# Kernel optimization log

Hardware: AMD Instinct MI355X
Metric: run time of the kernel (lower is better)

The kernel has to match this reference:

```python
import math
import jax, jax.numpy as jnp
import numpy as np

B, N, D, H, NI, NL, NS, MID = 32, 2048, 256, 8, 64, 3, 32, 3


def _ln(x, g, b, eps=1e-5):
    m = jnp.mean(x, axis=-1, keepdims=True)
    v = jnp.mean((x - m) ** 2, axis=-1, keepdims=True)
    return (x - m) * jax.lax.rsqrt(v + eps) * g + b


def _mab(Q, K, mask, Wq, bq, Wk, bk, Wv, bv, Wo, bo, g0, b0, g1, b1):
    # torch's split(dim_split,2)+cat(...,0) == reshape to (B, n, H, dh)
    dh = D // H
    q = (Q @ Wq + bq).reshape(Q.shape[0], Q.shape[1], H, dh)
    k = (K @ Wk + bk).reshape(K.shape[0], K.shape[1], H, dh)
    v = (K @ Wv + bv).reshape(K.shape[0], K.shape[1], H, dh)
    A = jnp.einsum('bqhd,bkhd->bhqk', q, k) / math.sqrt(D)  # note: sqrt(dim_V), faithful
    A = jnp.where(mask[:, None, None, :] == 0, -1e4, A)
    A = jax.nn.softmax(A, axis=-1)
    o = q + jnp.einsum('bhqk,bkhd->bqhd', A, v)
    O = o.reshape(Q.shape[0], Q.shape[1], D)
    O = _ln(O, g0, b0)
    O = O + jax.nn.relu(O @ Wo + bo)
    return _ln(O, g1, b1)


def _forward(x_values, y_target, point_mask, proj_W, proj_b, isab_I,
             isab_Wq, isab_bq, isab_Wk, isab_bk, isab_Wv, isab_bv,
             isab_Wo, isab_bo, isab_g0, isab_b0, isab_g1, isab_b1,
             pma_S, pma_Wq, pma_bq, pma_Wk, pma_bk, pma_Wv, pma_bv,
             pma_Wo, pma_bo, pma_g0, pma_b0, pma_g1, pma_b1):
    # input_dim == max_input_dim, so the zero-padded feature build is a concat
    feats = jnp.concatenate([x_values, y_target[..., None]], axis=-1)  # (B, N, MID+1)
    x = jax.nn.gelu(feats @ proj_W + proj_b, approximate=False)
    ones_mask = jnp.ones((x.shape[0], NI), jnp.float32)
    stk = (isab_Wq, isab_bq, isab_Wk, isab_bk, isab_Wv, isab_bv,
           isab_Wo, isab_bo, isab_g0, isab_b0, isab_g1, isab_b1)
    for l in range(NL):
        I = jnp.broadcast_to(isab_I[l][None], (x.shape[0], NI, D))
        h = _mab(I, x, point_mask, *[a[l, 0] for a in stk])   # mab0: inducing pts attend to X
        x = _mab(x, h, ones_mask, *[a[l, 1] for a in stk])    # mab1: X attends to H (all valid)
    S = jnp.broadcast_to(pma_S[None], (x.shape[0], NS, D))
    return _mab(S, x, point_mask, pma_Wq, pma_bq, pma_Wk, pma_bk, pma_Wv,
                pma_bv, pma_Wo, pma_bo, pma_g0, pma_b0, pma_g1, pma_b1)


def setup_inputs():
    key = jax.random.key(0)
    ks = iter(jax.random.split(key, 40))
    def nrm(shape, s=0.05):
        return jax.random.normal(next(ks), shape, dtype=jnp.float32) * s
    z = lambda shape: jnp.zeros(shape, jnp.float32)
    o = lambda shape: jnp.ones(shape, jnp.float32)
    return {
        'x_values': jax.random.normal(next(ks), (B, N, MID), jnp.float32),
        'y_target': jax.random.normal(next(ks), (B, N), jnp.float32),
        'point_mask': jax.random.randint(next(ks), (B, N), 0, 2).astype(jnp.float32),
        'proj_W': nrm((MID + 1, D)), 'proj_b': z((D,)),
        'isab_I': nrm((NL, NI, D), 0.1),
        'isab_Wq': nrm((NL, 2, D, D)), 'isab_bq': z((NL, 2, D)),
        'isab_Wk': nrm((NL, 2, D, D)), 'isab_bk': z((NL, 2, D)),
        'isab_Wv': nrm((NL, 2, D, D)), 'isab_bv': z((NL, 2, D)),
        'isab_Wo': nrm((NL, 2, D, D)), 'isab_bo': z((NL, 2, D)),
        'isab_g0': o((NL, 2, D)), 'isab_b0': z((NL, 2, D)),
        'isab_g1': o((NL, 2, D)), 'isab_b1': z((NL, 2, D)),
        'pma_S': nrm((NS, D), 0.1),
        'pma_Wq': nrm((D, D)), 'pma_bq': z((D,)),
        'pma_Wk': nrm((D, D)), 'pma_bk': z((D,)),
        'pma_Wv': nrm((D, D)), 'pma_bv': z((D,)),
        'pma_Wo': nrm((D, D)), 'pma_bo': z((D,)),
        'pma_g0': o((D,)), 'pma_b0': z((D,)),
        'pma_g1': o((D,)), 'pma_b1': z((D,)),
    }


def reference(x_values, y_target, point_mask, proj_W, proj_b, isab_I,
              isab_Wq, isab_bq, isab_Wk, isab_bk, isab_Wv, isab_bv,
              isab_Wo, isab_bo, isab_g0, isab_b0, isab_g1, isab_b1,
              pma_S, pma_Wq, pma_bq, pma_Wk, pma_bk, pma_Wv, pma_bv,
              pma_Wo, pma_bo, pma_g0, pma_b0, pma_g1, pma_b1):
    return _forward(x_values, y_target, point_mask, proj_W, proj_b, isab_I,
                    isab_Wq, isab_bq, isab_Wk, isab_bk, isab_Wv, isab_bv,
                    isab_Wo, isab_bo, isab_g0, isab_b0, isab_g1, isab_b1,
                    pma_S, pma_Wq, pma_bq, pma_Wk, pma_bk, pma_Wv, pma_bv,
                    pma_Wo, pma_bo, pma_g0, pma_b0, pma_g1, pma_b1)
```

## Files before the change

kernel.cpp:

```cpp
#include <hip/hip_runtime.h>
#include <hip/hip_bf16.h>


typedef __attribute__((ext_vector_type(8))) short short8;
typedef __attribute__((ext_vector_type(4))) float f32x4;
typedef __attribute__((ext_vector_type(4))) ushort ushort4v;

__device__ __forceinline__ ushort f2bf(float f) {
  uint u = __builtin_bit_cast(uint, f);
  u += 0x7fffu + ((u >> 16) & 1u);
  return (ushort)(u >> 16);
}
__device__ __forceinline__ float bf2f(ushort h) {
  uint u = (uint)h << 16;
  return __builtin_bit_cast(float, u);
}

__global__ __launch_bounds__(256) void prep_weights(
    const float* __restrict__ Wq, const float* __restrict__ Wk,
    const float* __restrict__ Wv, const float* __restrict__ Wo,
    const float* __restrict__ pWq, const float* __restrict__ pWk,
    const float* __restrict__ pWv, const float* __restrict__ pWo,
    ushort* __restrict__ wt)
{
  __shared__ float tile[64][65];
  const int m = blockIdx.y;
  const int t = blockIdx.x;
  const int tr = (t >> 2) * 64;
  const int tc = (t & 3) * 64;
  const float* src;
  if (m < 24) {
    int l = m >> 3, s = (m >> 2) & 1, w = m & 3;
    const float* base = (w == 0) ? Wq : (w == 1) ? Wk : (w == 2) ? Wv : Wo;
    src = base + (size_t)(l * 2 + s) * 65536;
  } else {
    int w = m & 3;
    src = (w == 0) ? pWq : (w == 1) ? pWk : (w == 2) ? pWv : pWo;
  }
  const int tid = threadIdx.x;
  const int cn = tid & 63;
  const int rk = tid >> 6;
#pragma unroll
  for (int j = 0; j < 16; ++j) {
    int kl = rk + j * 4;
    tile[kl][cn] = src[(size_t)(tr + kl) * 256 + tc + cn];
  }
  __syncthreads();
  ushort* dst = wt + (size_t)m * 65536;
#pragma unroll
  for (int j = 0; j < 16; ++j) {
    int nl = rk + j * 4;
    dst[(size_t)(tc + nl) * 256 + tr + cn] = f2bf(tile[cn][nl]);
  }
}

__global__ __launch_bounds__(256) void proj_gelu(
    const float* __restrict__ xv, const float* __restrict__ yt,
    const float* __restrict__ pW, const float* __restrict__ pb,
    ushort* __restrict__ xb)
{
  const int d = threadIdx.x;
  const int row0 = blockIdx.x * 8;
  const float w0 = pW[d], w1 = pW[256 + d], w2 = pW[512 + d], w3 = pW[768 + d];
  const float bz = pb[d];
#pragma unroll
  for (int rr = 0; rr < 8; ++rr) {
    int row = row0 + rr;
    float f0 = xv[(size_t)row * 3 + 0];
    float f1 = xv[(size_t)row * 3 + 1];
    float f2 = xv[(size_t)row * 3 + 2];
    float f3 = yt[row];
    float a = bz + f0 * w0 + f1 * w1 + f2 * w2 + f3 * w3;
    float g = 0.5f * a * (1.f + erff(a * 0.70710678118654752f));
    xb[(size_t)row * 256 + d] = f2bf(g);
  }
}

__global__ __launch_bounds__(256) void gemm_q(
    const float* __restrict__ iI, const float* __restrict__ pS,
    const ushort* __restrict__ wt, const float* __restrict__ ibq,
    const float* __restrict__ pbq, ushort* __restrict__ q_all)
{
  const int bq = blockIdx.x;
  const float* A; const ushort* Wt; const float* bias; ushort* out; int M;
  if (bq < 3) { A = iI + bq * 16384; Wt = wt + (size_t)(bq * 8) * 65536; bias = ibq + bq * 512; out = q_all + bq * 16384; M = 64; }
  else        { A = pS; Wt = wt + (size_t)24 * 65536; bias = pbq; out = q_all + 49152; M = 32; }
  const int tid = threadIdx.x;
  const int wave = tid >> 6, lane = tid & 63;
  const int l15 = lane & 15, l4 = lane >> 4, koff = l4 * 8;
  f32x4 acc[4][4];
#pragma unroll
  for (int i = 0; i < 4; ++i)
#pragma unroll
    for (int j = 0; j < 4; ++j) acc[i][j] = (f32x4)0.f;
#pragma unroll
  for (int ks = 0; ks < 8; ++ks) {
    short8 af[4];
#pragma unroll
    for (int mf = 0; mf < 4; ++mf) {
      if (mf * 16 < M) {
        const float* ap = A + (size_t)(mf * 16 + l15) * 256 + ks * 32 + koff;
        float4 f0 = *(const float4*)ap;
        float4 f1 = *(const float4*)(ap + 4);
        short8 sv;
        sv[0] = (short)f2bf(f0.x); sv[1] = (short)f2bf(f0.y);
        sv[2] = (short)f2bf(f0.z); sv[3] = (short)f2bf(f0.w);
        sv[4] = (short)f2bf(f1.x); sv[5] = (short)f2bf(f1.y);
        sv[6] = (short)f2bf(f1.z); sv[7] = (short)f2bf(f1.w);
        af[mf] = sv;
      } else af[mf] = (short8)0;
    }
#pragma unroll
    for (int nf = 0; nf < 4; ++nf) {
      short8 bf = *(const short8*)(Wt + (size_t)(wave * 64 + nf * 16 + l15) * 256 + ks * 32 + koff);
#pragma unroll
      for (int mf = 0; mf < 4; ++mf)
        acc[mf][nf] = __builtin_amdgcn_mfma_f32_16x16x32_bf16(af[mf], bf, acc[mf][nf], 0, 0, 0);
    }
  }
#pragma unroll
  for (int mf = 0; mf < 4; ++mf) {
    if (mf * 16 >= M) continue;
#pragma unroll
    for (int nf = 0; nf < 4; ++nf) {
      int col = wave * 64 + nf * 16 + l15;
      float bcol = bias[col];
#pragma unroll
      for (int r = 0; r < 4; ++r)
        out[(size_t)(mf * 16 + l4 * 4 + r) * 256 + col] = f2bf(acc[mf][nf][r] + bcol);
    }
  }
}

template <int EPI, bool OUTF32, int COLS>
__global__ __launch_bounds__(COLS * 2, (COLS == 128) ? 4 : 2) void gemm_bp(
    const ushort* __restrict__ A,
    const ushort* __restrict__ Wt0, const ushort* __restrict__ Wt1, const ushort* __restrict__ Wt2,
    const float* __restrict__ b0, const float* __restrict__ b1, const float* __restrict__ b2,
    void* __restrict__ o0, void* __restrict__ o1, void* __restrict__ o2,
    const float* __restrict__ lng, const float* __restrict__ lnb,
    int ny, int nyz)
{
  constexpr int WC = COLS / 64;
  constexpr int PS = COLS * 64;
  constexpr int ROWB = COLS * 2;
  __shared__ __align__(16) char Bs[4 * PS];
  __shared__ float redbuf[(EPI == 3) ? 1280 : 4];
  const int bid = blockIdx.x;
  const int rest = bid >> 3;
  const int yz = rest % nyz;
  const int bx = ((rest / nyz) << 3) | (bid & 7);
  const int y = yz % ny;
  const int z = yz / ny;
  const ushort* Wt = (z == 0) ? Wt0 : ((z == 1) ? Wt1 : Wt2);
  const float* bias = (z == 0) ? b0 : ((z == 1) ? b1 : b2);
  void* outp = (z == 0) ? o0 : ((z == 1) ? o1 : o2);
  const int pcol = y * COLS;

  const int tid = threadIdx.x;
  const int wave = tid >> 6, lane = tid & 63;
  const int wc = wave % WC, wr = wave / WC;
  const int l15 = lane & 15, l4 = lane >> 4;
  const int row0 = bx * 128;
  const int sn = tid >> 1, sseg = tid & 1;

  f32x4 acc[4][4];
#pragma unroll
  for (int i = 0; i < 4; ++i)
#pragma unroll
    for (int j = 0; j < 4; ++j) acc[i][j] = (f32x4)0.f;

#pragma unroll
  for (int half = 0; half < 2; ++half) {
    if (half) __syncthreads();
    {
      const ushort* src = Wt + (size_t)(pcol + sn) * 256 + half * 128 + sseg * 64;
#pragma unroll
      for (int c = 0; c < 8; ++c) {
        uint4 w = *(const uint4*)(src + c * 8);
        int plane = sseg * 2 + (c >> 2);
        char* dst = Bs + plane * PS + sn * 64 + (((c & 3) * 16) ^ (((sn >> 1) & 3) << 4));
        *(uint4*)dst = w;
      }
    }
    __syncthreads();
#pragma unroll
    for (int ks = 0; ks < 4; ++ks) {
      short8 af[4];
#pragma unroll
      for (int mfa = 0; mfa < 4; ++mfa)
        af[mfa] = *(const short8*)(A + (size_t)(row0 + wr * 64 + mfa * 16 + l15) * 256 + half * 128 + ks * 32 + l4 * 8);
#pragma unroll
      for (int nfb = 0; nfb < 4; ++nfb) {
        int n = wc * 64 + nfb * 16 + l15;
        short8 bf = *(const short8*)(Bs + ks * PS + n * 64 + ((l4 * 16) ^ (((n >> 1) & 3) << 4)));
#pragma unroll
        for (int mfa = 0; mfa < 4; ++mfa)
          acc[mfa][nfb] = __builtin_amdgcn_mfma_f32_16x16x32_bf16(bf, af[mfa], acc[mfa][nfb], 0, 0, 0);
      }
    }
  }

  if constexpr (EPI == 0) {
    __syncthreads();
#pragma unroll
    for (int nfb = 0; nfb < 4; ++nfb) {
      f32x4 bv = *(const f32x4*)(bias + pcol + wc * 64 + nfb * 16 + l4 * 4);
      int colb = wc * 128 + nfb * 32 + l4 * 8;
#pragma unroll
      for (int mfa = 0; mfa < 4; ++mfa) {
        int row = wr * 64 + mfa * 16 + l15;
        ushort4v pk;
#pragma unroll
        for (int i = 0; i < 4; ++i) pk[i] = f2bf(acc[mfa][nfb][i] + bv[i]);
        *(ushort4v*)(Bs + row * ROWB + (colb ^ ((row & 7) << 4))) = pk;
      }
    }
    __syncthreads();
    const int srow = tid >> 2, seg = tid & 3;
#pragma unroll
    for (int rr = 0; rr < 2; ++rr) {
      int row = srow + rr * 64;
      int x = (row & 7) << 4;
      ushort* gdst = (ushort*)outp + (size_t)(row0 + row) * 256 + pcol;
#pragma unroll
      for (int it = 0; it < 4; ++it) {
        int colb = seg * 16 + it * 64;
        uint4 v = *(const uint4*)(Bs + row * ROWB + (colb ^ x));
        *(uint4*)(gdst + colb / 2) = v;
      }
    }
  } else {
    float* red1 = redbuf;
    float* red2 = redbuf + 512;
    float* mv_ = redbuf + 1024;
    float* rv_ = redbuf + 1152;
    float s1[4] = {0.f, 0.f, 0.f, 0.f}, s2[4] = {0.f, 0.f, 0.f, 0.f};
#pragma unroll
    for (int nfb = 0; nfb < 4; ++nfb) {
      int col0 = wc * 64 + nfb * 16 + l4 * 4;
      f32x4 bv = *(const f32x4*)(bias + col0);
#pragma unroll
      for (int mfa = 0; mfa < 4; ++mfa) {
        size_t row = (size_t)row0 + wr * 64 + mfa * 16 + l15;
        ushort4v rz = *(const ushort4v*)(A + row * 256 + col0);
#pragma unroll
        for (int i = 0; i < 4; ++i) {
          float zz = bf2f(rz[i]) + fmaxf(acc[mfa][nfb][i] + bv[i], 0.f);
          acc[mfa][nfb][i] = zz;
          s1[mfa] += zz;
          s2[mfa] += zz * zz;
        }
      }
    }
#pragma unroll
    for (int mfa = 0; mfa < 4; ++mfa) {
      s1[mfa] += __shfl_xor(s1[mfa], 16); s1[mfa] += __shfl_xor(s1[mfa], 32);
      s2[mfa] += __shfl_xor(s2[mfa], 16); s2[mfa] += __shfl_xor(s2[mfa], 32);
    }
    if (l4 == 0) {
#pragma unroll
      for (int mfa = 0; mfa < 4; ++mfa) {
        red1[wc * 128 + wr * 64 + mfa * 16 + l15] = s1[mfa];
        red2[wc * 128 + wr * 64 + mfa * 16 + l15] = s2[mfa];
      }
    }
    __syncthreads();
    if (tid < 128) {
      float m1 = red1[tid] + red1[128 + tid] + red1[256 + tid] + red1[384 + tid];
      float m2 = red2[tid] + red2[128 + tid] + red2[256 + tid] + red2[384 + tid];
      float mean = m1 * 0.00390625f;
      float var = m2 * 0.00390625f - mean * mean;
      mv_[tid] = mean;
      rv_[tid] = rsqrtf(var + 1e-5f);
    }
    __syncthreads();
#pragma unroll
    for (int nfb = 0; nfb < 4; ++nfb) {
      int col0 = wc * 64 + nfb * 16 + l4 * 4;
      f32x4 gg = *(const f32x4*)(lng + col0);
      f32x4 bb = *(const f32x4*)(lnb + col0);
      int colb = col0 * 2;
#pragma unroll
      for (int mfa = 0; mfa < 4; ++mfa) {
        int lr = wr * 64 + mfa * 16 + l15;
        float mean = mv_[lr], rs = rv_[lr];
        if constexpr (OUTF32) {
          f32x4 w;
#pragma unroll
          for (int i = 0; i < 4; ++i) w[i] = (acc[mfa][nfb][i] - mean) * rs * gg[i] + bb[i];
          *(f32x4*)((float*)outp + ((size_t)row0 + lr) * 256 + col0) = w;
        } else {
          ushort4v pk;
#pragma unroll
          for (int i = 0; i < 4; ++i) pk[i] = f2bf((acc[mfa][nfb][i] - mean) * rs * gg[i] + bb[i]);
          *(ushort4v*)(Bs + lr * ROWB + (colb ^ ((lr & 7) << 4))) = pk;
        }
      }
    }
    if constexpr (!OUTF32) {
      __syncthreads();
      const int srow = tid >> 2, seg = tid & 3;
      int x = (srow & 7) << 4;
      ushort* gdst = (ushort*)outp + (size_t)(row0 + srow) * 256;
#pragma unroll
      for (int it = 0; it < 8; ++it) {
        int colb = seg * 16 + it * 64;
        uint4 v = *(const uint4*)(Bs + srow * ROWB + (colb ^ x));
        *(uint4*)(gdst + colb / 2) = v;
      }
    }
  }
}

template <int MF>
__global__ __launch_bounds__(512) void attn_fused(
    const ushort* __restrict__ qb, const ushort* __restrict__ xbuf,
    const ushort* __restrict__ wk, const float* __restrict__ bk,
    const ushort* __restrict__ wv, const float* __restrict__ bv,
    const float* __restrict__ mask, ushort* __restrict__ O)
{
  __shared__ __align__(16) ushort Ps[8][64][72];
  __shared__ __align__(16) ushort Vt[8][32][72];
  __shared__ __align__(16) ushort Kc[8][64][40];
  const int b = blockIdx.x, h = blockIdx.y;
  const int tid = threadIdx.x;
  const int w = tid >> 6, lane = tid & 63;
  const int l15 = lane & 15, l4 = lane >> 4;
  const int koff = l4 * 8;
  const int kvbase = b * 2048;

  short8 qf[MF];
#pragma unroll
  for (int mf = 0; mf < MF; ++mf)
    qf[mf] = *(const short8*)(qb + (size_t)(mf * 16 + l15) * 256 + h * 32 + koff);

  f32x4 bkv[2], bvv[2];
#pragma unroll
  for (int nfb = 0; nfb < 2; ++nfb) {
    bkv[nfb] = *(const f32x4*)(bk + h * 32 + nfb * 16 + l4 * 4);
    bvv[nfb] = *(const f32x4*)(bv + h * 32 + nfb * 16 + l4 * 4);
  }

  f32x4 Oa[MF][2];
  float Mr[MF][4], Lr[MF][4];
#pragma unroll
  for (int mf = 0; mf < MF; ++mf) {
    Oa[mf][0] = (f32x4)0.f; Oa[mf][1] = (f32x4)0.f;
#pragma unroll
    for (int r = 0; r < 4; ++r) { Mr[mf][r] = -1e30f; Lr[mf][r] = 0.f; }
  }

  for (int c = 0; c < 4; ++c) {
    const int kc = w * 256 + c * 64;
    f32x4 ak[4][2], av[4][2];
#pragma unroll
    for (int i = 0; i < 4; ++i) {
      ak[i][0] = (f32x4)0.f; ak[i][1] = (f32x4)0.f;
      av[i][0] = (f32x4)0.f; av[i][1] = (f32x4)0.f;
    }
#pragma unroll
    for (int ks = 0; ks < 8; ++ks) {
      short8 af[4];
#pragma unroll
      for (int mfa = 0; mfa < 4; ++mfa)
        af[mfa] = *(const short8*)(xbuf + (size_t)(kvbase + kc + mfa * 16 + l15) * 256 + ks * 32 + koff);
#pragma unroll
      for (int nfb = 0; nfb < 2; ++nfb) {
        int n = h * 32 + nfb * 16 + l15;
        short8 wkf = *(const short8*)(wk + (size_t)n * 256 + ks * 32 + koff);
        short8 wvf = *(const short8*)(wv + (size_t)n * 256 + ks * 32 + koff);
#pragma unroll
        for (int mfa = 0; mfa < 4; ++mfa) {
          ak[mfa][nfb] = __builtin_amdgcn_mfma_f32_16x16x32_bf16(wkf, af[mfa], ak[mfa][nfb], 0, 0, 0);
          av[mfa][nfb] = __builtin_amdgcn_mfma_f32_16x16x32_bf16(wvf, af[mfa], av[mfa][nfb], 0, 0, 0);
        }
      }
    }
#pragma unroll
    for (int nfb = 0; nfb < 2; ++nfb)
#pragma unroll
      for (int mfa = 0; mfa < 4; ++mfa) {
        ushort4v pk;
#pragma unroll
        for (int i = 0; i < 4; ++i) pk[i] = f2bf(ak[mfa][nfb][i] + bkv[nfb][i]);
        *(ushort4v*)&Kc[w][mfa * 16 + l15][nfb * 16 + l4 * 4] = pk;
      }
#pragma unroll
    for (int nfb = 0; nfb < 2; ++nfb)
#pragma unroll
      for (int mfa = 0; mfa < 4; ++mfa)
#pragma unroll
        for (int i = 0; i < 4; ++i)
          Vt[w][nfb * 16 + l4 * 4 + i][mfa * 16 + l15] = f2bf(av[mfa][nfb][i] + bvv[nfb][i]);

    f32x4 S[MF][4];
#pragma unroll
    for (int nf = 0; nf < 4; ++nf) {
      short8 kf = *(const short8*)&Kc[w][nf * 16 + l15][koff];
#pragma unroll
      for (int mf = 0; mf < MF; ++mf)
        S[mf][nf] = __builtin_amdgcn_mfma_f32_16x16x32_bf16(qf[mf], kf, (f32x4)0.f, 0, 0, 0);
    }
    float mv[4];
#pragma unroll
    for (int nf = 0; nf < 4; ++nf)
      mv[nf] = mask[(size_t)b * 2048 + kc + nf * 16 + l15];
#pragma unroll
    for (int mf = 0; mf < MF; ++mf)
#pragma unroll
      for (int nf = 0; nf < 4; ++nf)
#pragma unroll
        for (int r = 0; r < 4; ++r) {
          float s = S[mf][nf][r] * 0.0625f;
          S[mf][nf][r] = (mv[nf] != 0.f) ? s : -1e4f;
        }
#pragma unroll
    for (int mf = 0; mf < MF; ++mf)
#pragma unroll
      for (int r = 0; r < 4; ++r) {
        float pm = fmaxf(fmaxf(S[mf][0][r], S[mf][1][r]), fmaxf(S[mf][2][r], S[mf][3][r]));
        pm = fmaxf(pm, __shfl_xor(pm, 1));
        pm = fmaxf(pm, __shfl_xor(pm, 2));
        pm = fmaxf(pm, __shfl_xor(pm, 4));
        pm = fmaxf(pm, __shfl_xor(pm, 8));
        float Mnew = fmaxf(Mr[mf][r], pm);
        float corr = __expf(Mr[mf][r] - Mnew);
        Mr[mf][r] = Mnew;
        float rs = 0.f;
#pragma unroll
        for (int nf = 0; nf < 4; ++nf) {
          float p = __expf(S[mf][nf][r] - Mnew);
          S[mf][nf][r] = p;
          rs += p;
        }
        rs += __shfl_xor(rs, 1);
        rs += __shfl_xor(rs, 2);
        rs += __shfl_xor(rs, 4);
        rs += __shfl_xor(rs, 8);
        Lr[mf][r] = Lr[mf][r] * corr + rs;
        Oa[mf][0][r] *= corr;
        Oa[mf][1][r] *= corr;
      }
#pragma unroll
    for (int mf = 0; mf < MF; ++mf)
#pragma unroll
      for (int nf = 0; nf < 4; ++nf)
#pragma unroll
        for (int r = 0; r < 4; ++r)
          Ps[w][mf * 16 + l4 * 4 + r][nf * 16 + l15] = f2bf(S[mf][nf][r]);
#pragma unroll
    for (int ks = 0; ks < 2; ++ks) {
      short8 pf[MF];
#pragma unroll
      for (int mf = 0; mf < MF; ++mf)
        pf[mf] = *(const short8*)&Ps[w][mf * 16 + l15][ks * 32 + koff];
#pragma unroll
      for (int nf2 = 0; nf2 < 2; ++nf2) {
        short8 vf = *(const short8*)&Vt[w][nf2 * 16 + l15][ks * 32 + koff];
#pragma unroll
        for (int mf = 0; mf < MF; ++mf)
          Oa[mf][nf2] = __builtin_amdgcn_mfma_f32_16x16x32_bf16(pf[mf], vf, Oa[mf][nf2], 0, 0, 0);
      }
    }
  }

  __syncthreads();
  float* Mw = (float*)&Ps[0][0][0];
  float* Lw = Mw + 512;
  float* Ow = Lw + 512;
#pragma unroll
  for (int mf = 0; mf < MF; ++mf)
#pragma unroll
    for (int r = 0; r < 4; ++r) {
      int row = mf * 16 + l4 * 4 + r;
      if (l15 == 0) { Mw[w * 64 + row] = Mr[mf][r]; Lw[w * 64 + row] = Lr[mf][r]; }
#pragma unroll
      for (int nf2 = 0; nf2 < 2; ++nf2)
        Ow[(w * 64 + row) * 33 + nf2 * 16 + l15] = Oa[mf][nf2][r];
    }
  __syncthreads();
  const int NQ = MF * 16;
  int row = tid >> 3, dg = tid & 7;
  if (row < NQ) {
    float mm = -1e30f;
#pragma unroll
    for (int s = 0; s < 8; ++s) mm = fmaxf(mm, Mw[s * 64 + row]);
    float den = 0.f, es[8];
#pragma unroll
    for (int s = 0; s < 8; ++s) {
      es[s] = __expf(Mw[s * 64 + row] - mm);
      den += Lw[s * 64 + row] * es[s];
    }
    float invden = 1.f / den;
    ushort4v pk;
#pragma unroll
    for (int i = 0; i < 4; ++i) {
      int d = dg * 4 + i;
      float num = 0.f;
#pragma unroll
      for (int s = 0; s < 8; ++s) num += Ow[(s * 64 + row) * 33 + d] * es[s];
      float qv = bf2f(qb[(size_t)row * 256 + h * 32 + d]);
      pk[i] = f2bf(qv + num * invden);
    }
    *(ushort4v*)(O + (size_t)(b * NQ + row) * 256 + h * 32 + dg * 4) = pk;
  }
}

__global__ __launch_bounds__(512, 4) void mab1_fused(
    const ushort* __restrict__ xb, const ushort* __restrict__ wq,
    const float* __restrict__ bq,
    const ushort* __restrict__ kb, const ushort* __restrict__ vb,
    const ushort* __restrict__ wo, const float* __restrict__ bo,
    const float* __restrict__ g0, const float* __restrict__ b0v,
    const float* __restrict__ g1, const float* __restrict__ b1v,
    ushort* __restrict__ outb)
{
  __shared__ __align__(16) ushort Qs[8][64][40];
  __shared__ __align__(16) ushort Psh[8][16][40];
  __shared__ __align__(16) ushort Vth[8][32][40];
  __shared__ float red1[8][64], red2[8][64], mv_[64], rv_[64];
  ushort* o_s = &Qs[0][0][0];
  constexpr int OS = 264;

  const int qt = blockIdx.x, b = blockIdx.y;
  const int tid = threadIdx.x;
  const int w = tid >> 6, lane = tid & 63;
  const int l15 = lane & 15, l4 = lane >> 4;
  const int koff = l4 * 8;
  const size_t row0 = (size_t)b * 2048 + qt * 64;
  const int kvbase = b * 64;
  const int h = w;

  short8 kf[4];
#pragma unroll
  for (int nf = 0; nf < 4; ++nf)
    kf[nf] = *(const short8*)(kb + (size_t)(kvbase + nf * 16 + l15) * 256 + h * 32 + koff);
  const int key = lane & 31, dh2 = lane >> 5;
  short8 vvB0, vvB1;
  {
    const ushort* vsrcA = vb + (size_t)(kvbase + key) * 256 + h * 32 + dh2 * 16;
    const ushort* vsrcB = vb + (size_t)(kvbase + 32 + key) * 256 + h * 32 + dh2 * 16;
    short8 vvA0 = *(const short8*)vsrcA;
    short8 vvA1 = *(const short8*)(vsrcA + 8);
    vvB0 = *(const short8*)vsrcB;
    vvB1 = *(const short8*)(vsrcB + 8);
#pragma unroll
    for (int j = 0; j < 8; ++j) Vth[w][dh2 * 16 + j][key] = (ushort)vvA0[j];
#pragma unroll
    for (int j = 0; j < 8; ++j) Vth[w][dh2 * 16 + 8 + j][key] = (ushort)vvA1[j];
  }

  {
    f32x4 qa[4][2];
#pragma unroll
    for (int i = 0; i < 4; ++i) { qa[i][0] = (f32x4)0.f; qa[i][1] = (f32x4)0.f; }
#pragma unroll
    for (int ks = 0; ks < 8; ++ks) {
      short8 af[4];
#pragma unroll
      for (int mfa = 0; mfa < 4; ++mfa)
        af[mfa] = *(const short8*)(xb + (row0 + mfa * 16 + l15) * 256 + ks * 32 + koff);
#pragma unroll
      for (int nfb = 0; nfb < 2; ++nfb) {
        int n = w * 32 + nfb * 16 + l15;
        short8 bf = *(const short8*)(wq + (size_t)n * 256 + ks * 32 + koff);
#pragma unroll
        for (int mfa = 0; mfa < 4; ++mfa)
          qa[mfa][nfb] = __builtin_amdgcn_mfma_f32_16x16x32_bf16(bf, af[mfa], qa[mfa][nfb], 0, 0, 0);
      }
    }
#pragma unroll
    for (int nfb = 0; nfb < 2; ++nfb) {
      f32x4 bvq = *(const f32x4*)(bq + w * 32 + nfb * 16 + l4 * 4);
#pragma unroll
      for (int mfa = 0; mfa < 4; ++mfa) {
        ushort4v pk;
#pragma unroll
        for (int i = 0; i < 4; ++i) pk[i] = f2bf(qa[mfa][nfb][i] + bvq[i]);
        *(ushort4v*)&Qs[w][mfa * 16 + l15][nfb * 16 + l4 * 4] = pk;
      }
    }
  }

  short8 qf[4];
#pragma unroll
  for (int mf = 0; mf < 4; ++mf)
    qf[mf] = *(const short8*)&Qs[w][mf * 16 + l15][koff];

  f32x4 S[4][4];
#pragma unroll
  for (int nf = 0; nf < 4; ++nf) {
#pragma unroll
    for (int mf = 0; mf < 4; ++mf)
      S[mf][nf] = __builtin_amdgcn_mfma_f32_16x16x32_bf16(qf[mf], kf[nf], (f32x4)0.f, 0, 0, 0);
  }
  float Lr[4][4];
#pragma unroll
  for (int mf = 0; mf < 4; ++mf)
#pragma unroll
    for (int r = 0; r < 4; ++r) {
      float pm = fmaxf(fmaxf(S[mf][0][r], S[mf][1][r]), fmaxf(S[mf][2][r], S[mf][3][r])) * 0.0625f;
      pm = fmaxf(pm, __shfl_xor(pm, 1));
      pm = fmaxf(pm, __shfl_xor(pm, 2));
      pm = fmaxf(pm, __shfl_xor(pm, 4));
      pm = fmaxf(pm, __shfl_xor(pm, 8));
      float rs = 0.f;
#pragma unroll
      for (int nf = 0; nf < 4; ++nf) {
        float p = __expf(S[mf][nf][r] * 0.0625f - pm);
        S[mf][nf][r] = p;
        rs += p;
      }
      rs += __shfl_xor(rs, 1);
      rs += __shfl_xor(rs, 2);
      rs += __shfl_xor(rs, 4);
      rs += __shfl_xor(rs, 8);
      Lr[mf][r] = rs;
    }

  f32x4 Oa[4][2];
#pragma unroll
  for (int mf = 0; mf < 4; ++mf) { Oa[mf][0] = (f32x4)0.f; Oa[mf][1] = (f32x4)0.f; }
#pragma unroll
  for (int mf = 0; mf < 4; ++mf) {
#pragma unroll
    for (int nf = 0; nf < 2; ++nf)
#pragma unroll
      for (int r = 0; r < 4; ++r)
        Psh[w][l4 * 4 + r][nf * 16 + l15] = f2bf(S[mf][nf][r]);
    short8 pf = *(const short8*)&Psh[w][l15][koff];
#pragma unroll
    for (int nf2 = 0; nf2 < 2; ++nf2) {
      short8 vf = *(const short8*)&Vth[w][nf2 * 16 + l15][koff];
      Oa[mf][nf2] = __builtin_amdgcn_mfma_f32_16x16x32_bf16(pf, vf, Oa[mf][nf2], 0, 0, 0);
    }
  }
#pragma unroll
  for (int j = 0; j < 8; ++j) Vth[w][dh2 * 16 + j][key] = (ushort)vvB0[j];
#pragma unroll
  for (int j = 0; j < 8; ++j) Vth[w][dh2 * 16 + 8 + j][key] = (ushort)vvB1[j];
#pragma unroll
  for (int mf = 0; mf < 4; ++mf) {
#pragma unroll
    for (int nf = 0; nf < 2; ++nf)
#pragma unroll
      for (int r = 0; r < 4; ++r)
        Psh[w][l4 * 4 + r][nf * 16 + l15] = f2bf(S[mf][nf + 2][r]);
    short8 pf = *(const short8*)&Psh[w][l15][koff];
#pragma unroll
    for (int nf2 = 0; nf2 < 2; ++nf2) {
      short8 vf = *(const short8*)&Vth[w][nf2 * 16 + l15][koff];
      Oa[mf][nf2] = __builtin_amdgcn_mfma_f32_16x16x32_bf16(pf, vf, Oa[mf][nf2], 0, 0, 0);
    }
  }

  {
    float s1[4][4], s2[4][4];
#pragma unroll
    for (int mf = 0; mf < 4; ++mf)
#pragma unroll
      for (int r = 0; r < 4; ++r) {
        float invL = 1.f / Lr[mf][r];
        s1[mf][r] = 0.f; s2[mf][r] = 0.f;
#pragma unroll
        for (int nf2 = 0; nf2 < 2; ++nf2) {
          float qv = bf2f(Qs[w][mf * 16 + l4 * 4 + r][nf2 * 16 + l15]);
          float z = qv + Oa[mf][nf2][r] * invL;
          Oa[mf][nf2][r] = z;
          s1[mf][r] += z;
          s2[mf][r] += z * z;
        }
#pragma unroll
        for (int off = 1; off < 16; off <<= 1) {
          s1[mf][r] += __shfl_xor(s1[mf][r], off);
          s2[mf][r] += __shfl_xor(s2[mf][r], off);
        }
        if (l15 == 0) {
          int row = mf * 16 + l4 * 4 + r;
          red1[w][row] = s1[mf][r];
          red2[w][row] = s2[mf][r];
        }
      }
  }
  __syncthreads();
  if (tid < 64) {
    float m1 = 0.f, m2 = 0.f;
#pragma unroll
    for (int s = 0; s < 8; ++s) { m1 += red1[s][tid]; m2 += red2[s][tid]; }
    float mean = m1 * 0.00390625f;
    float var = m2 * 0.00390625f - mean * mean;
    mv_[tid] = mean;
    rv_[tid] = rsqrtf(var + 1e-5f);
  }
  __syncthreads();
#pragma unroll
  for (int nf2 = 0; nf2 < 2; ++nf2) {
    int col = h * 32 + nf2 * 16 + l15;
    float gc = g0[col], bc = b0v[col];
#pragma unroll
    for (int mf = 0; mf < 4; ++mf)
#pragma unroll
      for (int r = 0; r < 4; ++r) {
        int row = mf * 16 + l4 * 4 + r;
        float v = (Oa[mf][nf2][r] - mv_[row]) * rv_[row] * gc + bc;
        o_s[row * OS + col] = f2bf(v);
      }
  }
  __syncthreads();

  f32x4 oa[4][2];
#pragma unroll
  for (int i = 0; i < 4; ++i) { oa[i][0] = (f32x4)0.f; oa[i][1] = (f32x4)0.f; }
#pragma unroll
  for (int ks = 0; ks < 8; ++ks) {
    short8 af[4];
#pragma unroll
    for (int mfa = 0; mfa < 4; ++mfa)
      af[mfa] = *(const short8*)&o_s[(mfa * 16 + l15) * OS + ks * 32 + koff];
#pragma unroll
    for (int nfb = 0; nfb < 2; ++nfb) {
      int n = w * 32 + nfb * 16 + l15;
      short8 bf = *(const short8*)(wo + (size_t)n * 256 + ks * 32 + koff);
#pragma unroll
      for (int mfa = 0; mfa < 4; ++mfa)
        oa[mfa][nfb] = __builtin_amdgcn_mfma_f32_16x16x32_bf16(bf, af[mfa], oa[mfa][nfb], 0, 0, 0);
    }
  }
  float t1[4] = {0.f, 0.f, 0.f, 0.f}, t2[4] = {0.f, 0.f, 0.f, 0.f};
#pragma unroll
  for (int nfb = 0; nfb < 2; ++nfb) {
    int col0 = w * 32 + nfb * 16 + l4 * 4;
    f32x4 bvo = *(const f32x4*)(bo + col0);
#pragma unroll
    for (int mfa = 0; mfa < 4; ++mfa) {
      int row = mfa * 16 + l15;
      ushort4v rz = *(const ushort4v*)&o_s[row * OS + col0];
#pragma unroll
      for (int i = 0; i < 4; ++i) {
        float zz = bf2f(rz[i]) + fmaxf(oa[mfa][nfb][i] + bvo[i], 0.f);
        oa[mfa][nfb][i] = zz;
        t1[mfa] += zz;
        t2[mfa] += zz * zz;
      }
    }
  }
#pragma unroll
  for (int mfa = 0; mfa < 4; ++mfa) {
    t1[mfa] += __shfl_xor(t1[mfa], 16); t1[mfa] += __shfl_xor(t1[mfa], 32);
    t2[mfa] += __shfl_xor(t2[mfa], 16); t2[mfa] += __shfl_xor(t2[mfa], 32);
  }
  if (l4 == 0) {
#pragma unroll
    for (int mfa = 0; mfa < 4; ++mfa) {
      red1[w][mfa * 16 + l15] = t1[mfa];
      red2[w][mfa * 16 + l15] = t2[mfa];
    }
  }
  __syncthreads();
  if (tid < 64) {
    float m1 = 0.f, m2 = 0.f;
#pragma unroll
    for (int s = 0; s < 8; ++s) { m1 += red1[s][tid]; m2 += red2[s][tid]; }
    float mean = m1 * 0.00390625f;
    float var = m2 * 0.00390625f - mean * mean;
    mv_[tid] = mean;
    rv_[tid] = rsqrtf(var + 1e-5f);
  }
  __syncthreads();
#pragma unroll
  for (int nfb = 0; nfb < 2; ++nfb) {
    int col0 = w * 32 + nfb * 16 + l4 * 4;
    f32x4 gg = *(const f32x4*)(g1 + col0);
    f32x4 bb = *(const f32x4*)(b1v + col0);
#pragma unroll
    for (int mfa = 0; mfa < 4; ++mfa) {
      int row = mfa * 16 + l15;
      ushort4v pk;
#pragma unroll
      for (int i = 0; i < 4; ++i)
        pk[i] = f2bf((oa[mfa][nfb][i] - mv_[row]) * rv_[row] * gg[i] + bb[i]);
      *(ushort4v*)&o_s[row * OS + col0] = pk;
    }
  }
  __syncthreads();
  {
    const int r_ = tid >> 3, sg = tid & 7;
    ushort* gdst = outb + (row0 + r_) * 256 + sg * 32;
    const ushort* src = &o_s[r_ * OS + sg * 32];
#pragma unroll
    for (int it = 0; it < 4; ++it) {
      uint4 v = *(const uint4*)(src + it * 8);
      *(uint4*)(gdst + it * 8) = v;
    }
  }
}

__global__ __launch_bounds__(256) void ln4(
    const ushort* __restrict__ in, ushort* __restrict__ out,
    const float* __restrict__ g, const float* __restrict__ bb)
{
  const int w = threadIdx.x >> 6, lane = threadIdx.x & 63;
  const size_t row = (size_t)blockIdx.x * 4 + w;
  ushort4v u = *(const ushort4v*)(in + row * 256 + lane * 4);
  float v[4];
#pragma unroll
  for (int i = 0; i < 4; ++i) v[i] = bf2f(u[i]);
  float s1 = v[0] + v[1] + v[2] + v[3];
  float s2 = v[0] * v[0] + v[1] * v[1] + v[2] * v[2] + v[3] * v[3];
#pragma unroll
  for (int off = 1; off < 64; off <<= 1) {
    s1 += __shfl_xor(s1, off);
    s2 += __shfl_xor(s2, off);
  }
  float mean = s1 * 0.00390625f;
  float var = s2 * 0.00390625f - mean * mean;
  float rs = rsqrtf(var + 1e-5f);
  f32x4 gg = *(const f32x4*)(g + lane * 4);
  f32x4 bv = *(const f32x4*)(bb + lane * 4);
  ushort4v p;
#pragma unroll
  for (int i = 0; i < 4; ++i) p[i] = f2bf((v[i] - mean) * rs * gg[i] + bv[i]);
  *(ushort4v*)(out + row * 256 + lane * 4) = p;
}

extern "C" void kernel_launch(void* const* d_in, const int* in_sizes, int n_in,
                              void* d_out, int out_size, void* d_ws, size_t ws_size,
                              hipStream_t stream) {
  const float* xv = (const float*)d_in[0];
  const float* yt = (const float*)d_in[1];
  const float* pmask = (const float*)d_in[2];
  const float* prW = (const float*)d_in[3];
  const float* prb = (const float*)d_in[4];
  const float* iI = (const float*)d_in[5];
  const float* iWq = (const float*)d_in[6];
  const float* ibq = (const float*)d_in[7];
  const float* iWk = (const float*)d_in[8];
  const float* ibk = (const float*)d_in[9];
  const float* iWv = (const float*)d_in[10];
  const float* ibv = (const float*)d_in[11];
  const float* iWo = (const float*)d_in[12];
  const float* ibo = (const float*)d_in[13];
  const float* ig0 = (const float*)d_in[14];
  const float* ib0 = (const float*)d_in[15];
  const float* ig1 = (const float*)d_in[16];
  const float* ib1 = (const float*)d_in[17];
  const float* pS = (const float*)d_in[18];
  const float* pWq = (const float*)d_in[19];
  const float* pbq = (const float*)d_in[20];
  const float* pWk = (const float*)d_in[21];
  const float* pbk = (const float*)d_in[22];
  const float* pWv = (const float*)d_in[23];
  const float* pbv = (const float*)d_in[24];
  const float* pWo = (const float*)d_in[25];
  const float* pbo = (const float*)d_in[26];
  const float* pg0 = (const float*)d_in[27];
  const float* pb0 = (const float*)d_in[28];
  const float* pg1 = (const float*)d_in[29];
  const float* pb1 = (const float*)d_in[30];

  char* ws = (char*)d_ws;
  if (ws_size < 172621824u) return;
  ushort* xb = (ushort*)(ws + 0);
  ushort* ob = (ushort*)(ws + 33554432);
  ushort* hb = (ushort*)(ws + 67108864);
  ushort* kbw = (ushort*)(ws + 101711872);
  ushort* vbw = (ushort*)(ws + 135266304);
  ushort* wt = (ushort*)(ws + 168820736);
  ushort* q_all = (ushort*)(ws + 172490752);

  prep_weights<<<dim3(16, 28), 256, 0, stream>>>(iWq, iWk, iWv, iWo, pWq, pWk, pWv, pWo, wt);
  proj_gelu<<<8192, 256, 0, stream>>>(xv, yt, prW, prb, xb);
  gemm_q<<<4, 256, 0, stream>>>(iI, pS, wt, ibq, pbq, q_all);

  for (int l = 0; l < 3; ++l) {
    const int s0 = l * 2, s1 = l * 2 + 1;
    const ushort* wk = wt + (size_t)(l * 8 + 1) * 65536;
    const ushort* wv = wt + (size_t)(l * 8 + 2) * 65536;
    const ushort* wo0 = wt + (size_t)(l * 8 + 3) * 65536;
    const ushort* wq1 = wt + (size_t)(l * 8 + 4) * 65536;
    const ushort* wk1 = wt + (size_t)(l * 8 + 5) * 65536;
    const ushort* wv1 = wt + (size_t)(l * 8 + 6) * 65536;
    const ushort* wo1 = wt + (size_t)(l * 8 + 7) * 65536;
    attn_fused<4><<<dim3(32, 8), 512, 0, stream>>>(
        q_all + l * 16384, xb, wk, ibk + s0 * 256, wv, ibv + s0 * 256, pmask, ob);
    ln4<<<512, 256, 0, stream>>>(ob, ob, ig0 + s0 * 256, ib0 + s0 * 256);
    gemm_bp<3, false, 256><<<16, 512, 0, stream>>>(
        ob, wo0, wo0, wo0, ibo + s0 * 256, ibo + s0 * 256, ibo + s0 * 256,
        hb, hb, hb, ig1 + s0 * 256, ib1 + s0 * 256, 1, 1);
    gemm_bp<0, false, 128><<<64, 256, 0, stream>>>(
        hb, wk1, wv1, wv1, ibk + s1 * 256, ibv + s1 * 256, ibv + s1 * 256,
        kbw, vbw, vbw, nullptr, nullptr, 2, 4);
    mab1_fused<<<dim3(32, 32), 512, 0, stream>>>(
        xb, wq1, ibq + s1 * 256, kbw, vbw, wo1, ibo + s1 * 256,
        ig0 + s1 * 256, ib0 + s1 * 256, ig1 + s1 * 256, ib1 + s1 * 256, xb);
  }
  attn_fused<2><<<dim3(32, 8), 512, 0, stream>>>(
      q_all + 49152, xb, wt + (size_t)25 * 65536, pbk, wt + (size_t)26 * 65536, pbv, pmask, ob);
  ln4<<<256, 256, 0, stream>>>(ob, ob, pg0, pb0);
  gemm_bp<3, true, 256><<<8, 512, 0, stream>>>(
      ob, wt + (size_t)27 * 65536, wt + (size_t)27 * 65536, wt + (size_t)27 * 65536,
      pbo, pbo, pbo, d_out, d_out, d_out, pg1, pb1, 1, 1);
}
```

Baseline: 793.0 us.

## Split mab0 attention by key range across blocks, merge partials in separate kernel

The fused attention kernel used to give each block one (batch, head) with its 8 waves splitting the keys, then merged the partial softmax results in shared memory. Now each block owns a 256-key range for one batch and its 8 waves take the 8 heads. All heads in a block then read the same x rows, so those loads are shared through cache. Partial O/M/L values go to global scratch and a new attn_merge kernel combines them. The K staging buffer also shrinks to one 16-row tile per wave. In exchange there is an extra launch and global round-trip traffic for the partials.

```diff
diff --git a/kernel.cpp b/kernel.cpp
--- a/kernel.cpp
+++ b/kernel.cpp
@@ -314,21 +314,24 @@
 }
 
 template <int MF>
-__global__ __launch_bounds__(512) void attn_fused(
+__global__ __launch_bounds__(512) void attn_split(
     const ushort* __restrict__ qb, const ushort* __restrict__ xbuf,
     const ushort* __restrict__ wk, const float* __restrict__ bk,
     const ushort* __restrict__ wv, const float* __restrict__ bv,
-    const float* __restrict__ mask, ushort* __restrict__ O)
+    const float* __restrict__ mask,
+    float* __restrict__ Opart, float* __restrict__ Mpart, float* __restrict__ Lpart)
 {
   __shared__ __align__(16) ushort Ps[8][64][72];
   __shared__ __align__(16) ushort Vt[8][32][72];
-  __shared__ __align__(16) ushort Kc[8][64][40];
-  const int b = blockIdx.x, h = blockIdx.y;
+  __shared__ __align__(16) ushort Kc16[8][16][40];
+  const int b = blockIdx.x, kr = blockIdx.y;
   const int tid = threadIdx.x;
   const int w = tid >> 6, lane = tid & 63;
   const int l15 = lane & 15, l4 = lane >> 4;
   const int koff = l4 * 8;
   const int kvbase = b * 2048;
+  const int h = w;
+  const int p = (b * 8 + h) * 8 + kr;
 
   short8 qf[MF];
 #pragma unroll
@@ -352,7 +355,7 @@
   }
 
   for (int c = 0; c < 4; ++c) {
-    const int kc = w * 256 + c * 64;
+    const int kc = kr * 256 + c * 64;
     f32x4 ak[4][2], av[4][2];
 #pragma unroll
     for (int i = 0; i < 4; ++i) {
@@ -380,15 +383,6 @@
 #pragma unroll
     for (int nfb = 0; nfb < 2; ++nfb)
 #pragma unroll
-      for (int mfa = 0; mfa < 4; ++mfa) {
-        ushort4v pk;
-#pragma unroll
-        for (int i = 0; i < 4; ++i) pk[i] = f2bf(ak[mfa][nfb][i] + bkv[nfb][i]);
-        *(ushort4v*)&Kc[w][mfa * 16 + l15][nfb * 16 + l4 * 4] = pk;
-      }
-#pragma unroll
-    for (int nfb = 0; nfb < 2; ++nfb)
-#pragma unroll
       for (int mfa = 0; mfa < 4; ++mfa)
 #pragma unroll
         for (int i = 0; i < 4; ++i)
@@ -397,7 +391,14 @@
     f32x4 S[MF][4];
 #pragma unroll
     for (int nf = 0; nf < 4; ++nf) {
-      short8 kf = *(const short8*)&Kc[w][nf * 16 + l15][koff];
+#pragma unroll
+      for (int nfb = 0; nfb < 2; ++nfb) {
+        ushort4v pk;
+#pragma unroll
+        for (int i = 0; i < 4; ++i) pk[i] = f2bf(ak[nf][nfb][i] + bkv[nfb][i]);
+        *(ushort4v*)&Kc16[w][l15][nfb * 16 + l4 * 4] = pk;
+      }
+      short8 kf = *(const short8*)&Kc16[w][l15][koff];
 #pragma unroll
       for (int mf = 0; mf < MF; ++mf)
         S[mf][nf] = __builtin_amdgcn_mfma_f32_16x16x32_bf16(qf[mf], kf, (f32x4)0.f, 0, 0, 0);
@@ -430,9 +431,9 @@
         float rs = 0.f;
 #pragma unroll
         for (int nf = 0; nf < 4; ++nf) {
-          float p = __expf(S[mf][nf][r] - Mnew);
-          S[mf][nf][r] = p;
-          rs += p;
+          float pp = __expf(S[mf][nf][r] - Mnew);
+          S[mf][nf][r] = pp;
+          rs += pp;
         }
         rs += __shfl_xor(rs, 1);
         rs += __shfl_xor(rs, 2);
@@ -465,46 +466,57 @@
     }
   }
 
-  __syncthreads();
-  float* Mw = (float*)&Ps[0][0][0];
-  float* Lw = Mw + 512;
-  float* Ow = Lw + 512;
 #pragma unroll
   for (int mf = 0; mf < MF; ++mf)
 #pragma unroll
     for (int r = 0; r < 4; ++r) {
       int row = mf * 16 + l4 * 4 + r;
-      if (l15 == 0) { Mw[w * 64 + row] = Mr[mf][r]; Lw[w * 64 + row] = Lr[mf][r]; }
+      if (l15 == 0) {
+        Mpart[(size_t)p * 64 + row] = Mr[mf][r];
+        Lpart[(size_t)p * 64 + row] = Lr[mf][r];
+      }
 #pragma unroll
       for (int nf2 = 0; nf2 < 2; ++nf2)
-        Ow[(w * 64 + row) * 33 + nf2 * 16 + l15] = Oa[mf][nf2][r];
-    }
-  __syncthreads();
+        Opart[(size_t)p * 2048 + row * 32 + nf2 * 16 + l15] = Oa[mf][nf2][r];
+    }
+}
+
+template <int MF>
+__global__ __launch_bounds__(256) void attn_merge(
+    const ushort* __restrict__ qb, const float* __restrict__ Opart,
+    const float* __restrict__ Mpart, const float* __restrict__ Lpart,
+    ushort* __restrict__ O)
+{
+  const int b = blockIdx.x, h = blockIdx.y;
+  const int tid = threadIdx.x;
   const int NQ = MF * 16;
-  int row = tid >> 3, dg = tid & 7;
-  if (row < NQ) {
-    float mm = -1e30f;
-#pragma unroll
-    for (int s = 0; s < 8; ++s) mm = fmaxf(mm, Mw[s * 64 + row]);
-    float den = 0.f, es[8];
-#pragma unroll
-    for (int s = 0; s < 8; ++s) {
-      es[s] = __expf(Mw[s * 64 + row] - mm);
-      den += Lw[s * 64 + row] * es[s];
-    }
-    float invden = 1.f / den;
-    ushort4v pk;
-#pragma unroll
-    for (int i = 0; i < 4; ++i) {
-      int d = dg * 4 + i;
-      float num = 0.f;
-#pragma unroll
-      for (int s = 0; s < 8; ++s) num += Ow[(s * 64 + row) * 33 + d] * es[s];
-      float qv = bf2f(qb[(size_t)row * 256 + h * 32 + d]);
-      pk[i] = f2bf(qv + num * invden);
-    }
-    *(ushort4v*)(O + (size_t)(b * NQ + row) * 256 + h * 32 + dg * 4) = pk;
-  }
+  const int row = tid >> 2, dg = tid & 3;
+  if (row >= NQ) return;
+  const size_t pb = ((size_t)(b * 8 + h)) * 8;
+  float mm = -1e30f;
+#pragma unroll
+  for (int s = 0; s < 8; ++s) mm = fmaxf(mm, Mpart[(pb + s) * 64 + row]);
+  float den = 0.f, es[8];
+#pragma unroll
+  for (int s = 0; s < 8; ++s) {
+    es[s] = __expf(Mpart[(pb + s) * 64 + row] - mm);
+    den += Lpart[(pb + s) * 64 + row] * es[s];
+  }
+  float invden = 1.f / den;
+  ushort4v pk0, pk1;
+#pragma unroll
+  for (int i = 0; i < 8; ++i) {
+    int d = dg * 8 + i;
+    float num = 0.f;
+#pragma unroll
+    for (int s = 0; s < 8; ++s) num += Opart[(pb + s) * 2048 + row * 32 + d] * es[s];
+    float qv = bf2f(qb[(size_t)row * 256 + h * 32 + d]);
+    ushort res = f2bf(qv + num * invden);
+    if (i < 4) pk0[i] = res; else pk1[i - 4] = res;
+  }
+  ushort* dst = O + (size_t)(b * NQ + row) * 256 + h * 32 + dg * 8;
+  *(ushort4v*)dst = pk0;
+  *(ushort4v*)(dst + 4) = pk1;
 }
 
 __global__ __launch_bounds__(512, 4) void mab1_fused(
@@ -608,9 +620,9 @@
       float rs = 0.f;
 #pragma unroll
       for (int nf = 0; nf < 4; ++nf) {
-        float p = __expf(S[mf][nf][r] * 0.0625f - pm);
-        S[mf][nf][r] = p;
-        rs += p;
+        float pp = __expf(S[mf][nf][r] * 0.0625f - pm);
+        S[mf][nf][r] = pp;
+        rs += pp;
       }
       rs += __shfl_xor(rs, 1);
       rs += __shfl_xor(rs, 2);
@@ -868,6 +880,9 @@
   ushort* vbw = (ushort*)(ws + 135266304);
   ushort* wt = (ushort*)(ws + 168820736);
   ushort* q_all = (ushort*)(ws + 172490752);
+  float* Opart = (float*)(ws + 101711872);
+  float* Mpart = (float*)(ws + 101711872 + 16777216);
+  float* Lpart = Mpart + 131072;
 
   prep_weights<<<dim3(16, 28), 256, 0, stream>>>(iWq, iWk, iWv, iWo, pWq, pWk, pWv, pWo, wt);
   proj_gelu<<<8192, 256, 0, stream>>>(xv, yt, prW, prb, xb);
@@ -882,8 +897,11 @@
     const ushort* wk1 = wt + (size_t)(l * 8 + 5) * 65536;
     const ushort* wv1 = wt + (size_t)(l * 8 + 6) * 65536;
     const ushort* wo1 = wt + (size_t)(l * 8 + 7) * 65536;
-    attn_fused<4><<<dim3(32, 8), 512, 0, stream>>>(
-        q_all + l * 16384, xb, wk, ibk + s0 * 256, wv, ibv + s0 * 256, pmask, ob);
+    attn_split<4><<<dim3(32, 8), 512, 0, stream>>>(
+        q_all + l * 16384, xb, wk, ibk + s0 * 256, wv, ibv + s0 * 256, pmask,
+        Opart, Mpart, Lpart);
+    attn_merge<4><<<dim3(32, 8), 256, 0, stream>>>(
+        q_all + l * 16384, Opart, Mpart, Lpart, ob);
     ln4<<<512, 256, 0, stream>>>(ob, ob, ig0 + s0 * 256, ib0 + s0 * 256);
     gemm_bp<3, false, 256><<<16, 512, 0, stream>>>(
         ob, wo0, wo0, wo0, ibo + s0 * 256, ibo + s0 * 256, ibo + s0 * 256,
@@ -895,8 +913,11 @@
         xb, wq1, ibq + s1 * 256, kbw, vbw, wo1, ibo + s1 * 256,
         ig0 + s1 * 256, ib0 + s1 * 256, ig1 + s1 * 256, ib1 + s1 * 256, xb);
   }
-  attn_fused<2><<<dim3(32, 8), 512, 0, stream>>>(
-      q_all + 49152, xb, wt + (size_t)25 * 65536, pbk, wt + (size_t)26 * 65536, pbv, pmask, ob);
+  attn_split<2><<<dim3(32, 8), 512, 0, stream>>>(
+      q_all + 49152, xb, wt + (size_t)25 * 65536, pbk, wt + (size_t)26 * 65536, pbv, pmask,
+      Opart, Mpart, Lpart);
+  attn_merge<2><<<dim3(32, 8), 256, 0, stream>>>(
+      q_all + 49152, Opart, Mpart, Lpart, ob);
   ln4<<<256, 256, 0, stream>>>(ob, ob, pg0, pb0);
   gemm_bp<3, true, 256><<<8, 512, 0, stream>>>(
       ob, wt + (size_t)27 * 65536, wt + (size_t)27 * 65536, wt + (size_t)27 * 65536,
```

Result: slower. 814.3 us (+2.7%).
